# Kernel tuning notes

Measured on AMD Instinct MI355X. Metric: run time of the kernel, lower is better.

Reference implementation:

```python
import jax, jax.numpy as jnp
import numpy as np

NUM_REL = 3


def _edge_norm(dst, et, n_nodes):
    # PyG RGCNConv default aggr='mean': mean over edges per (dst, relation).
    seg = dst * NUM_REL + et
    cnt = jax.ops.segment_sum(jnp.ones(dst.shape[0], jnp.float32), seg,
                              num_segments=n_nodes * NUM_REL)
    return 1.0 / jnp.maximum(cnt, 1.0)[seg], seg  # [E]


def _rgcn_layer(x, W, root, b, src, dst, et, norm_e, seg, transform_first):
    n = x.shape[0]
    if transform_first:
        # h_r = x @ W_r for all relations, gather message per edge, scatter-add.
        H = jnp.einsum('ni,rio->rno', x, W)          # [R, N, out]
        m = H[et, src] * norm_e[:, None]             # [E, out]
        agg = jax.ops.segment_sum(m, dst, num_segments=n)
    else:
        # mean-aggregate in input space first (mean commutes with linear map).
        m = x[src] * norm_e[:, None]                 # [E, in]
        A = jax.ops.segment_sum(m, seg, num_segments=n * NUM_REL)
        A = A.reshape(n, NUM_REL, -1)                # [N, R, in]
        agg = jnp.einsum('nri,rio->no', A, W)
    return agg + x @ root + b


def _make_params(key, in_c, out_c):
    dims = [(in_c, 1024), (1024, 512), (512, 128)]
    ks = jax.random.split(key, 14)
    p = {}
    for li, (i, o) in enumerate(dims, start=1):
        p[f'W{li}'] = jax.random.normal(ks[3 * li - 3], (NUM_REL, i, o), jnp.float32) * 0.02
        p[f'root{li}'] = jax.random.normal(ks[3 * li - 2], (i, o), jnp.float32) * 0.02
        p[f'b{li}'] = jnp.zeros((o,), jnp.float32)
    p['fc_w'] = jax.random.normal(ks[9], (128, out_c), jnp.float32) * 0.02
    p['fc_b'] = jnp.zeros((out_c,), jnp.float32)
    return p


def setup_inputs() -> dict:
    key = jax.random.key(0)
    N, E, IN_C, OUT_C = 40000, 500000, 256, 21
    k1, k2, k3, k4 = jax.random.split(key, 4)
    inp = {
        'x': jax.random.normal(k1, (N, IN_C), jnp.float32),
        'edge_index': jax.random.randint(k2, (2, E), 0, N, jnp.int64)
            if jax.config.jax_enable_x64 else jax.random.randint(k2, (2, E), 0, N, jnp.int32),
        'edge_type': jax.random.randint(k3, (E,), 0, NUM_REL, jnp.int32),
    }
    inp.update(_make_params(k4, IN_C, OUT_C))
    return inp


def reference(x, edge_index, edge_type, W1, root1, b1, W2, root2, b2,
              W3, root3, b3, fc_w, fc_b):
    src, dst = edge_index[0], edge_index[1]
    et = edge_type
    n = x.shape[0]
    norm_e, seg = _edge_norm(dst, et, n)
    # layer 1: in(256) < out(1024) -> aggregate-first is cheaper
    h = _rgcn_layer(x, W1, root1, b1, src, dst, et, norm_e, seg, transform_first=False)
    h = jax.nn.relu(h)  # dropout is identity in eval mode
    # layer 2: in(1024) > out(512) -> transform-first
    h = _rgcn_layer(h, W2, root2, b2, src, dst, et, norm_e, seg, transform_first=True)
    h = jax.nn.relu(h)
    # layer 3: in(512) > out(128) -> transform-first
    h = _rgcn_layer(h, W3, root3, b3, src, dst, et, norm_e, seg, transform_first=True)
    h = jax.nn.relu(h)
    logits = h @ fc_w + fc_b
    return jax.nn.log_softmax(logits, axis=1)
```

## Files before the change

kernel.cpp:

```cpp
#include <hip/hip_runtime.h>
#include <cstdint>
#include <cstddef>


typedef short bf16x8 __attribute__((ext_vector_type(8)));
typedef float f32x4 __attribute__((ext_vector_type(4)));

#define GF_BIAS 1
#define GF_RELU 2
#define GF_BF16 4

__device__ __forceinline__ unsigned short f2bf(float f) {
    unsigned u = __float_as_uint(f);
    return (unsigned short)((u + 0x7FFFu + ((u >> 16) & 1u)) >> 16);
}
__device__ __forceinline__ float bf2f(unsigned short h) {
    return __uint_as_float((unsigned)h << 16);
}

__global__ __launch_bounds__(256) void zero_kernel(float* __restrict__ p, long n4)
{
    long i = (long)blockIdx.x * 256 + threadIdx.x;
    if (i < n4) ((float4*)p)[i] = make_float4(0.f, 0.f, 0.f, 0.f);
}

__global__ __launch_bounds__(256) void count_kernel(
    const int* __restrict__ dst, const int* __restrict__ et,
    int* __restrict__ cnt, int E)
{
    int e = blockIdx.x * 256 + threadIdx.x;
    if (e < E) atomicAdd(&cnt[dst[e] * 3 + et[e]], 1);
}

__global__ __launch_bounds__(256) void scanA(
    const int* __restrict__ cnt, int* __restrict__ base,
    int* __restrict__ bsum, int S)
{
    __shared__ int sh[256];
    int i = blockIdx.x * 256 + threadIdx.x;
    int v = (i < S) ? cnt[i] : 0;
    sh[threadIdx.x] = v;
    __syncthreads();
#pragma unroll
    for (int off = 1; off < 256; off <<= 1) {
        int t = (threadIdx.x >= off) ? sh[threadIdx.x - off] : 0;
        __syncthreads();
        sh[threadIdx.x] += t;
        __syncthreads();
    }
    if (i < S) base[i] = sh[threadIdx.x] - v;
    if (threadIdx.x == 255) bsum[blockIdx.x] = sh[255];
}

__global__ __launch_bounds__(512) void scanB(int* __restrict__ bsum, int NB)
{
    __shared__ int sh[512];
    int t = threadIdx.x;
    int v = (t < NB) ? bsum[t] : 0;
    sh[t] = v;
    __syncthreads();
#pragma unroll
    for (int off = 1; off < 512; off <<= 1) {
        int u = (t >= off) ? sh[t - off] : 0;
        __syncthreads();
        sh[t] += u;
        __syncthreads();
    }
    if (t < NB) bsum[t] = sh[t] - v;
}

__global__ __launch_bounds__(256) void scanC(
    int* __restrict__ base, const int* __restrict__ bsum, int S)
{
    int i = blockIdx.x * 256 + threadIdx.x;
    if (i < S) base[i] += bsum[blockIdx.x];
}

__global__ __launch_bounds__(256) void fill_kernel(
    const int* __restrict__ src, const int* __restrict__ dst,
    const int* __restrict__ et, int* __restrict__ base,
    int* __restrict__ cnt, int* __restrict__ elist, int E, int S)
{
    int e = blockIdx.x * 256 + threadIdx.x;
    if (e == 0) base[S] = E;
    if (e >= E) return;
    int seg = dst[e] * 3 + et[e];
    int old = atomicSub(&cnt[seg], 1);
    elist[base[seg] + old - 1] = src[e];
}

__global__ __launch_bounds__(256) void tr1_tiled(
    const float* __restrict__ W1, const float* __restrict__ root1,
    unsigned short* __restrict__ W1t)
{
    __shared__ float sh[32][33];
    int bk = blockIdx.x & 31, bj = blockIdx.x >> 5;
    int tc = threadIdx.x & 31, tr = threadIdx.x >> 5;
    int k0 = bk * 32, j0 = bj * 32;
#pragma unroll
    for (int i = 0; i < 4; ++i) {
        int k = k0 + tr + i * 8;
        float v = (k < 768) ? W1[(size_t)k * 1024 + j0 + tc]
                            : root1[(size_t)(k - 768) * 1024 + j0 + tc];
        sh[tr + i * 8][tc] = v;
    }
    __syncthreads();
#pragma unroll
    for (int i = 0; i < 4; ++i)
        W1t[(size_t)(j0 + tr + i * 8) * 1024 + k0 + tc] = f2bf(sh[tc][tr + i * 8]);
}

__global__ __launch_bounds__(256) void tr2_tiled(
    const float* __restrict__ root2, const float* __restrict__ W2,
    unsigned short* __restrict__ W2cat)
{
    __shared__ float sh[32][33];
    int bk = blockIdx.x & 31, br = blockIdx.x >> 5;
    int tc = threadIdx.x & 31, tr = threadIdx.x >> 5;
    int k0 = bk * 32, r0 = br * 32;
    int s = r0 >> 9, j0 = r0 & 511;
    const float* src = (s == 0) ? root2 : W2 + (size_t)(s - 1) * 524288;
#pragma unroll
    for (int i = 0; i < 4; ++i)
        sh[tr + i * 8][tc] = src[(size_t)(k0 + tr + i * 8) * 512 + j0 + tc];
    __syncthreads();
#pragma unroll
    for (int i = 0; i < 4; ++i)
        W2cat[(size_t)(r0 + tr + i * 8) * 1024 + k0 + tc] = f2bf(sh[tc][tr + i * 8]);
}

__global__ __launch_bounds__(256) void tr3_tiled(
    const float* __restrict__ root3, const float* __restrict__ W3,
    unsigned short* __restrict__ W3cat)
{
    __shared__ float sh[32][33];
    int bk = blockIdx.x & 15, br = blockIdx.x >> 4;
    int tc = threadIdx.x & 31, tr = threadIdx.x >> 5;
    int k0 = bk * 32, r0 = br * 32;
    int s = r0 >> 7, j0 = r0 & 127;
    const float* src = (s == 0) ? root3 : W3 + (size_t)(s - 1) * 65536;
#pragma unroll
    for (int i = 0; i < 4; ++i)
        sh[tr + i * 8][tc] = src[(size_t)(k0 + tr + i * 8) * 128 + j0 + tc];
    __syncthreads();
#pragma unroll
    for (int i = 0; i < 4; ++i)
        W3cat[(size_t)(r0 + tr + i * 8) * 512 + k0 + tc] = f2bf(sh[tc][tr + i * 8]);
}

__global__ __launch_bounds__(256) void bias_cat(
    float* __restrict__ b2cat, float* __restrict__ b3cat,
    const float* __restrict__ b2, const float* __restrict__ b3)
{
    int i = blockIdx.x * 256 + threadIdx.x;
    if (i < 2048) b2cat[i] = (i < 512) ? b2[i] : 0.f;
    else if (i < 2560) { int j = i - 2048; b3cat[j] = (j < 128) ? b3[j] : 0.f; }
}

__global__ __launch_bounds__(256) void conv_bf16(
    const float* __restrict__ s, unsigned short* __restrict__ d, long n8)
{
    long i = (long)blockIdx.x * 256 + threadIdx.x;
    if (i >= n8) return;
    const float* p = s + i * 8;
    float4 a = *(const float4*)p, b = *(const float4*)(p + 4);
    ushort4 o0, o1;
    o0.x = f2bf(a.x); o0.y = f2bf(a.y); o0.z = f2bf(a.z); o0.w = f2bf(a.w);
    o1.x = f2bf(b.x); o1.y = f2bf(b.y); o1.z = f2bf(b.z); o1.w = f2bf(b.w);
    *(ushort4*)(d + i * 8) = o0;
    *(ushort4*)(d + i * 8 + 4) = o1;
}

__global__ __launch_bounds__(256) void agg1_kernel(
    const unsigned short* __restrict__ xb, const int* __restrict__ base,
    const int* __restrict__ elist, unsigned short* __restrict__ Xcat)
{
    int n = blockIdx.x;
    int w = threadIdx.x >> 6, l = threadIdx.x & 63;
    if (w == 3) {
        *(ushort4*)&Xcat[(size_t)n * 1024 + 768 + l * 4] =
            *(const ushort4*)&xb[(size_t)n * 256 + l * 4];
        return;
    }
    int seg = n * 3 + w;
    int st = base[seg], len = base[seg + 1] - st;
    float norm = 1.0f / (float)(len > 0 ? len : 1);
    int g = l >> 5, c8 = (l & 31) * 8;
    float a[8];
#pragma unroll
    for (int j = 0; j < 8; ++j) a[j] = 0.f;
    for (int i = g; i < len; i += 2) {
        const unsigned short* q = xb + (size_t)elist[st + i] * 256 + c8;
        ushort4 v0 = *(const ushort4*)q;
        ushort4 v1 = *(const ushort4*)(q + 4);
        a[0] += bf2f(v0.x); a[1] += bf2f(v0.y); a[2] += bf2f(v0.z); a[3] += bf2f(v0.w);
        a[4] += bf2f(v1.x); a[5] += bf2f(v1.y); a[6] += bf2f(v1.z); a[7] += bf2f(v1.w);
    }
#pragma unroll
    for (int j = 0; j < 8; ++j) a[j] += __shfl_xor(a[j], 32);
    if (l < 32) {
        ushort4 o0, o1;
        o0.x = f2bf(a[0] * norm); o0.y = f2bf(a[1] * norm);
        o0.z = f2bf(a[2] * norm); o0.w = f2bf(a[3] * norm);
        o1.x = f2bf(a[4] * norm); o1.y = f2bf(a[5] * norm);
        o1.z = f2bf(a[6] * norm); o1.w = f2bf(a[7] * norm);
        unsigned short* d = Xcat + (size_t)n * 1024 + w * 256 + c8;
        *(ushort4*)d = o0;
        *(ushort4*)(d + 4) = o1;
    }
}

__global__ __launch_bounds__(256) void agg2_fused(
    const unsigned short* __restrict__ H2all, unsigned short* __restrict__ h2b,
    const int* __restrict__ base, const int* __restrict__ elist)
{
    int w = threadIdx.x >> 6, l = threadIdx.x & 63;
    int n = blockIdx.x * 4 + w;
    int c8 = l * 8;
    const unsigned short* rowN = H2all + (size_t)n * 2048 + c8;
    float a[8];
    {
        ushort4 r0 = *(const ushort4*)rowN;
        ushort4 r1 = *(const ushort4*)(rowN + 4);
        a[0] = bf2f(r0.x); a[1] = bf2f(r0.y); a[2] = bf2f(r0.z); a[3] = bf2f(r0.w);
        a[4] = bf2f(r1.x); a[5] = bf2f(r1.y); a[6] = bf2f(r1.z); a[7] = bf2f(r1.w);
    }
    int s0 = base[n * 3], s1b = base[n * 3 + 1];
    int s2b = base[n * 3 + 2], s3 = base[n * 3 + 3];
    int l0 = s1b - s0, l1 = s2b - s1b, l2 = s3 - s2b;
    float nm0 = 1.f / (float)(l0 > 0 ? l0 : 1);
    float nm1 = 1.f / (float)(l1 > 0 ? l1 : 1);
    float nm2 = 1.f / (float)(l2 > 0 ? l2 : 1);
    int i = s0;
    for (; i + 2 <= s3; i += 2) {
        int ia = i, ib = i + 1;
        int ra = (ia >= s1b) + (ia >= s2b);
        int rb = (ib >= s1b) + (ib >= s2b);
        float wa = (ia < s1b) ? nm0 : ((ia < s2b) ? nm1 : nm2);
        float wb = (ib < s1b) ? nm0 : ((ib < s2b) ? nm1 : nm2);
        const unsigned short* qa =
            H2all + (size_t)elist[ia] * 2048 + 512 * (1 + ra) + c8;
        const unsigned short* qb =
            H2all + (size_t)elist[ib] * 2048 + 512 * (1 + rb) + c8;
        ushort4 u0 = *(const ushort4*)qa, u1 = *(const ushort4*)(qa + 4);
        ushort4 v0 = *(const ushort4*)qb, v1 = *(const ushort4*)(qb + 4);
        a[0] += bf2f(u0.x) * wa + bf2f(v0.x) * wb;
        a[1] += bf2f(u0.y) * wa + bf2f(v0.y) * wb;
        a[2] += bf2f(u0.z) * wa + bf2f(v0.z) * wb;
        a[3] += bf2f(u0.w) * wa + bf2f(v0.w) * wb;
        a[4] += bf2f(u1.x) * wa + bf2f(v1.x) * wb;
        a[5] += bf2f(u1.y) * wa + bf2f(v1.y) * wb;
        a[6] += bf2f(u1.z) * wa + bf2f(v1.z) * wb;
        a[7] += bf2f(u1.w) * wa + bf2f(v1.w) * wb;
    }
    if (i < s3) {
        int r = (i >= s1b) + (i >= s2b);
        float wN = (i < s1b) ? nm0 : ((i < s2b) ? nm1 : nm2);
        const unsigned short* q =
            H2all + (size_t)elist[i] * 2048 + 512 * (1 + r) + c8;
        ushort4 u0 = *(const ushort4*)q, u1 = *(const ushort4*)(q + 4);
        a[0] += bf2f(u0.x) * wN; a[1] += bf2f(u0.y) * wN;
        a[2] += bf2f(u0.z) * wN; a[3] += bf2f(u0.w) * wN;
        a[4] += bf2f(u1.x) * wN; a[5] += bf2f(u1.y) * wN;
        a[6] += bf2f(u1.z) * wN; a[7] += bf2f(u1.w) * wN;
    }
    ushort4 o0, o1;
    o0.x = f2bf(fmaxf(a[0], 0.f)); o0.y = f2bf(fmaxf(a[1], 0.f));
    o0.z = f2bf(fmaxf(a[2], 0.f)); o0.w = f2bf(fmaxf(a[3], 0.f));
    o1.x = f2bf(fmaxf(a[4], 0.f)); o1.y = f2bf(fmaxf(a[5], 0.f));
    o1.z = f2bf(fmaxf(a[6], 0.f)); o1.w = f2bf(fmaxf(a[7], 0.f));
    unsigned short* d = h2b + (size_t)n * 512 + c8;
    *(ushort4*)d = o0;
    *(ushort4*)(d + 4) = o1;
}

__global__ __launch_bounds__(256) void agg3_head(
    const unsigned short* __restrict__ H3cat, const float* __restrict__ fcw,
    const float* __restrict__ fcb, const int* __restrict__ base,
    const int* __restrict__ elist, float* __restrict__ out)
{
    __shared__ float sh[4][128];
    int wid = threadIdx.x >> 6, lane = threadIdx.x & 63;
    int n = blockIdx.x * 4 + wid;
    int g = lane >> 4, c8 = (lane & 15) * 8;
    int s0 = base[n * 3], s1b = base[n * 3 + 1];
    int s2b = base[n * 3 + 2], s3 = base[n * 3 + 3];
    int l0 = s1b - s0, l1 = s2b - s1b, l2 = s3 - s2b;
    float nm0 = 1.f / (float)(l0 > 0 ? l0 : 1);
    float nm1 = 1.f / (float)(l1 > 0 ? l1 : 1);
    float nm2 = 1.f / (float)(l2 > 0 ? l2 : 1);
    float a[8];
#pragma unroll
    for (int j = 0; j < 8; ++j) a[j] = 0.f;
    for (int i = s0 + g; i < s3; i += 4) {
        int r = (i >= s1b) + (i >= s2b);
        float wN = (i < s1b) ? nm0 : ((i < s2b) ? nm1 : nm2);
        const unsigned short* q =
            H3cat + (size_t)elist[i] * 512 + 128 * (1 + r) + c8;
        ushort4 u0 = *(const ushort4*)q, u1 = *(const ushort4*)(q + 4);
        a[0] += bf2f(u0.x) * wN; a[1] += bf2f(u0.y) * wN;
        a[2] += bf2f(u0.z) * wN; a[3] += bf2f(u0.w) * wN;
        a[4] += bf2f(u1.x) * wN; a[5] += bf2f(u1.y) * wN;
        a[6] += bf2f(u1.z) * wN; a[7] += bf2f(u1.w) * wN;
    }
#pragma unroll
    for (int j = 0; j < 8; ++j) {
        a[j] += __shfl_xor(a[j], 16);
        a[j] += __shfl_xor(a[j], 32);
    }
    if (lane < 16) {
        const unsigned short* rt = H3cat + (size_t)n * 512 + c8;
        ushort4 r0 = *(const ushort4*)rt, r1 = *(const ushort4*)(rt + 4);
        sh[wid][c8 + 0] = fmaxf(a[0] + bf2f(r0.x), 0.f);
        sh[wid][c8 + 1] = fmaxf(a[1] + bf2f(r0.y), 0.f);
        sh[wid][c8 + 2] = fmaxf(a[2] + bf2f(r0.z), 0.f);
        sh[wid][c8 + 3] = fmaxf(a[3] + bf2f(r0.w), 0.f);
        sh[wid][c8 + 4] = fmaxf(a[4] + bf2f(r1.x), 0.f);
        sh[wid][c8 + 5] = fmaxf(a[5] + bf2f(r1.y), 0.f);
        sh[wid][c8 + 6] = fmaxf(a[6] + bf2f(r1.z), 0.f);
        sh[wid][c8 + 7] = fmaxf(a[7] + bf2f(r1.w), 0.f);
    }
    __syncthreads();
    float logit = 0.f;
    if (lane < 21) {
        logit = fcb[lane];
#pragma unroll
        for (int k = 0; k < 128; ++k) logit += sh[wid][k] * fcw[k * 21 + lane];
    }
    float v = (lane < 21) ? logit : -INFINITY;
#pragma unroll
    for (int off = 32; off; off >>= 1) v = fmaxf(v, __shfl_xor(v, off));
    float mx = v;
    float ex = (lane < 21) ? expf(logit - mx) : 0.f;
#pragma unroll
    for (int off = 32; off; off >>= 1) ex += __shfl_xor(ex, off);
    if (lane < 21) out[(size_t)n * 21 + lane] = logit - mx - logf(ex);
}

__global__ __launch_bounds__(128) void agg2_inc(
    const unsigned short* __restrict__ H2q, float* __restrict__ h2acc,
    unsigned short* __restrict__ h2b, const int* __restrict__ base,
    const int* __restrict__ elist, int r, int last)
{
    int n = blockIdx.x, t = threadIdx.x;
    int seg = n * 3 + r;
    int st = base[seg], len = base[seg + 1] - st;
    float norm = 1.0f / (float)(len > 0 ? len : 1);
    float4 s = make_float4(0.f, 0.f, 0.f, 0.f);
    for (int i = 0; i < len; ++i) {
        int sx = elist[st + i];
        ushort4 v = *(const ushort4*)&H2q[(size_t)sx * 512 + t * 4];
        s.x += bf2f(v.x); s.y += bf2f(v.y); s.z += bf2f(v.z); s.w += bf2f(v.w);
    }
    float4 a = *(const float4*)&h2acc[(size_t)n * 512 + t * 4];
    a.x += s.x * norm; a.y += s.y * norm; a.z += s.z * norm; a.w += s.w * norm;
    if (!last) {
        *(float4*)&h2acc[(size_t)n * 512 + t * 4] = a;
    } else {
        ushort4 o;
        o.x = f2bf(fmaxf(a.x, 0.f)); o.y = f2bf(fmaxf(a.y, 0.f));
        o.z = f2bf(fmaxf(a.z, 0.f)); o.w = f2bf(fmaxf(a.w, 0.f));
        *(ushort4*)&h2b[(size_t)n * 512 + t * 4] = o;
    }
}

__global__ __launch_bounds__(256) void gemm_mfma(
    const unsigned short* __restrict__ A, const unsigned short* __restrict__ Bt,
    const float* __restrict__ bias, void* __restrict__ C,
    int Nout, int K, int flags, int lgGX)
{
    __shared__ short __align__(16) As[8192];
    __shared__ short __align__(16) Bs[8192];
    const int tid = threadIdx.x;
    const int w = tid >> 6, l = tid & 63;

    const int nblk = (int)gridDim.x;
    const int q = nblk >> 3, rem = nblk & 7;
    const int xcd = blockIdx.x & 7, local = blockIdx.x >> 3;
    const int id2 = xcd * q + (xcd < rem ? xcd : rem) + local;
    const int row0 = (id2 >> lgGX) * 128;
    const int col0 = (id2 & ((1 << lgGX) - 1)) * 128;

    const int wm = w >> 1, wn = w & 1;
    const int lr = l >> 3, lc = l & 7;

    f32x4 acc[4][4];
#pragma unroll
    for (int i = 0; i < 4; ++i)
#pragma unroll
        for (int j = 0; j < 4; ++j) acc[i][j] = (f32x4){0.f, 0.f, 0.f, 0.f};

    for (int k0 = 0; k0 < K; k0 += 64) {
        __syncthreads();
#pragma unroll
        for (int i = 0; i < 4; ++i) {
            const int c  = i * 4 + w;
            const int r  = c * 8 + lr;
            const int c8 = lc ^ (r & 7);
            __builtin_amdgcn_global_load_lds(
                (const __attribute__((address_space(1))) void*)
                    (A + (size_t)(row0 + r) * K + k0 + c8 * 8),
                (__attribute__((address_space(3))) void*)(As + c * 512),
                16, 0, 0);
            __builtin_amdgcn_global_load_lds(
                (const __attribute__((address_space(1))) void*)
                    (Bt + (size_t)(col0 + r) * K + k0 + c8 * 8),
                (__attribute__((address_space(3))) void*)(Bs + c * 512),
                16, 0, 0);
        }
        __syncthreads();
#pragma unroll
        for (int ks = 0; ks < 2; ++ks) {
            bf16x8 af[4], bfv[4];
#pragma unroll
            for (int mf = 0; mf < 4; ++mf) {
                int r = wm * 64 + mf * 16 + (l & 15);
                int byt = (r * 128 + ks * 64 + (l >> 4) * 16) ^ ((r & 7) << 4);
                af[mf] = *(const bf16x8*)((const char*)As + byt);
            }
#pragma unroll
            for (int nf = 0; nf < 4; ++nf) {
                int r = wn * 64 + nf * 16 + (l & 15);
                int byt = (r * 128 + ks * 64 + (l >> 4) * 16) ^ ((r & 7) << 4);
                bfv[nf] = *(const bf16x8*)((const char*)Bs + byt);
            }
#pragma unroll
            for (int mf = 0; mf < 4; ++mf)
#pragma unroll
                for (int nf = 0; nf < 4; ++nf)
                    acc[mf][nf] = __builtin_amdgcn_mfma_f32_16x16x32_bf16(
                        af[mf], bfv[nf], acc[mf][nf], 0, 0, 0);
        }
    }

    const int lrow = (l >> 4) * 4;
    const int lcol = l & 15;
#pragma unroll
    for (int mf = 0; mf < 4; ++mf) {
#pragma unroll
        for (int nf = 0; nf < 4; ++nf) {
            int col = col0 + wn * 64 + nf * 16 + lcol;
            float bv = (flags & GF_BIAS) ? bias[col] : 0.f;
#pragma unroll
            for (int rr = 0; rr < 4; ++rr) {
                int row = row0 + wm * 64 + mf * 16 + lrow + rr;
                float v = acc[mf][nf][rr] + bv;
                if (flags & GF_RELU) v = fmaxf(v, 0.f);
                size_t idx = (size_t)row * Nout + col;
                if (flags & GF_BF16) ((unsigned short*)C)[idx] = f2bf(v);
                else                 ((float*)C)[idx] = v;
            }
        }
    }
}

extern "C" void kernel_launch(void* const* d_in, const int* in_sizes, int n_in,
                              void* d_out, int out_size, void* d_ws, size_t ws_size,
                              hipStream_t stream)
{
    const float* x     = (const float*)d_in[0];
    const int*   ei    = (const int*)d_in[1];
    const int*   etp   = (const int*)d_in[2];
    const float* W1    = (const float*)d_in[3];
    const float* root1 = (const float*)d_in[4];
    const float* b1    = (const float*)d_in[5];
    const float* W2    = (const float*)d_in[6];
    const float* root2 = (const float*)d_in[7];
    const float* b2    = (const float*)d_in[8];
    const float* W3    = (const float*)d_in[9];
    const float* root3 = (const float*)d_in[10];
    const float* b3    = (const float*)d_in[11];
    const float* fcw   = (const float*)d_in[12];
    const float* fcb   = (const float*)d_in[13];
    float* out = (float*)d_out;
    (void)n_in; (void)out_size;

    const int N   = in_sizes[0] / 256;
    const int E   = in_sizes[2];
    const int S   = N * 3;
    const int NP  = (N + 127) / 128 * 128;
    const int GY  = NP / 128;
    const int NB  = (S + 255) / 256;
    const int* srcp = ei;
    const int* dstp = ei + E;

    const size_t SZ_X1024 = (size_t)NP * 1024 * 2;
    const size_t SZ_X512b = (size_t)NP * 512 * 2;
    const size_t SZ_X2048 = (size_t)NP * 2048 * 2;

    char* ws = (char*)d_ws;
    int*            cnt   = (int*)(ws + 0);
    int*            base  = (int*)(ws + 480256);
    int*            elist = (int*)(ws + 960512);
    float*          b2cat = (float*)(ws + 2960512);
    float*          b3cat = (float*)(ws + 2968704);
    unsigned short* W3cat = (unsigned short*)(ws + 2970752);
    unsigned short* W2cat = (unsigned short*)(ws + 3495040);
    const size_t fixed_end = 7689344;
    const size_t FUSED_NEED = 7692288 + SZ_X2048 + SZ_X1024;
    const bool fused = ws_size >= FUSED_NEED;

    char* arena;
    unsigned short *W1t, *xb, *Xcat, *h1b, *H2all, *H2q, *h2b, *H3cat;
    float* h2acc;
    if (fused) {
        arena = ws + 7692288;
        Xcat  = (unsigned short*)(arena);
        W1t   = (unsigned short*)(arena + SZ_X1024);
        xb    = (unsigned short*)(arena + SZ_X1024 + 2097152);
        h1b   = (unsigned short*)(arena + SZ_X2048);
        H2all = (unsigned short*)(arena);
        h2b   = (unsigned short*)(arena + SZ_X2048);
        H3cat = (unsigned short*)(arena);
        H2q = nullptr; h2acc = nullptr;
    } else {
        W1t   = (unsigned short*)(ws + fixed_end);
        arena = ws + 9789440;
        Xcat  = (unsigned short*)(arena);
        h2acc = (float*)(arena);
        h1b   = (unsigned short*)(arena + SZ_X1024);
        h2b   = (unsigned short*)(arena + SZ_X1024);
        H3cat = (unsigned short*)(arena + SZ_X1024 + SZ_X512b);
        xb    = (unsigned short*)(arena + 2 * SZ_X1024);
        H2q   = (unsigned short*)(arena + 2 * SZ_X1024);
        H2all = nullptr;
    }
    int* bsum = (int*)(arena);

    zero_kernel<<<(30016 + 255) / 256, 256, 0, stream>>>((float*)cnt, 30016);
    count_kernel<<<(E + 255) / 256, 256, 0, stream>>>(dstp, etp, cnt, E);
    scanA<<<NB, 256, 0, stream>>>(cnt, base, bsum, S);
    scanB<<<1, 512, 0, stream>>>(bsum, NB);
    scanC<<<NB, 256, 0, stream>>>(base, bsum, S);
    fill_kernel<<<(E + 255) / 256, 256, 0, stream>>>(srcp, dstp, etp, base, cnt, elist, E, S);

    tr1_tiled<<<1024, 256, 0, stream>>>(W1, root1, W1t);
    tr2_tiled<<<2048, 256, 0, stream>>>(root2, W2, W2cat);
    tr3_tiled<<<256, 256, 0, stream>>>(root3, W3, W3cat);
    bias_cat<<<10, 256, 0, stream>>>(b2cat, b3cat, b2, b3);
    conv_bf16<<<(int)(((long)N * 32 + 255) / 256), 256, 0, stream>>>(x, xb, (long)N * 32);

    agg1_kernel<<<N, 256, 0, stream>>>(xb, base, elist, Xcat);
    gemm_mfma<<<8 * GY, 256, 0, stream>>>(
        Xcat, W1t, b1, h1b, 1024, 1024, GF_BIAS | GF_RELU | GF_BF16, 3);

    if (fused) {
        gemm_mfma<<<16 * GY, 256, 0, stream>>>(
            h1b, W2cat, b2cat, H2all, 2048, 1024, GF_BIAS | GF_BF16, 4);
        agg2_fused<<<N / 4, 256, 0, stream>>>(H2all, h2b, base, elist);
    } else {
        gemm_mfma<<<4 * GY, 256, 0, stream>>>(
            h1b, W2cat, b2, h2acc, 512, 1024, GF_BIAS, 2);
        for (int r = 0; r < 3; ++r) {
            gemm_mfma<<<4 * GY, 256, 0, stream>>>(
                h1b, W2cat + (size_t)(1 + r) * 524288, nullptr, H2q, 512, 1024, GF_BF16, 2);
            agg2_inc<<<N, 128, 0, stream>>>(H2q, h2acc, h2b, base, elist, r, r == 2);
        }
    }

    gemm_mfma<<<4 * GY, 256, 0, stream>>>(
        h2b, W3cat, b3cat, H3cat, 512, 512, GF_BIAS | GF_BF16, 2);
    agg3_head<<<N / 4, 256, 0, stream>>>(H3cat, fcw, fcb, base, elist, out);
}
```

Measured before the change: 626.4 us.

## Merge weight-prep kernels into one launch and split agg2 edges across warps

Five small preparation kernels (three weight transposes, bias concatenation, x-to-bf16 conversion) become one kernel that branches on block index, which removes launch overhead. The layer-2 aggregation changes from one wave per node to one 256-thread block per node. The four waves stride over that node's edges, and their partial sums are reduced in shared memory before the root term, ReLU and bf16 store. This adds parallelism for nodes with many edges, at the cost of a block-wide sync and a shared-memory reduction per node.

Measured after the change: 619.0 us. About the same (-1.2%).

```diff
diff --git a/kernel.cpp b/kernel.cpp
--- a/kernel.cpp
+++ b/kernel.cpp
@@ -89,86 +89,75 @@
     elist[base[seg] + old - 1] = src[e];
 }
 
-__global__ __launch_bounds__(256) void tr1_tiled(
+__global__ __launch_bounds__(256) void prep_all(
     const float* __restrict__ W1, const float* __restrict__ root1,
-    unsigned short* __restrict__ W1t)
+    unsigned short* __restrict__ W1t,
+    const float* __restrict__ root2, const float* __restrict__ W2,
+    unsigned short* __restrict__ W2cat,
+    const float* __restrict__ root3, const float* __restrict__ W3,
+    unsigned short* __restrict__ W3cat,
+    float* __restrict__ b2cat, float* __restrict__ b3cat,
+    const float* __restrict__ b2, const float* __restrict__ b3,
+    const float* __restrict__ x, unsigned short* __restrict__ xb, long n8)
 {
     __shared__ float sh[32][33];
-    int bk = blockIdx.x & 31, bj = blockIdx.x >> 5;
+    int b = blockIdx.x;
     int tc = threadIdx.x & 31, tr = threadIdx.x >> 5;
-    int k0 = bk * 32, j0 = bj * 32;
-#pragma unroll
-    for (int i = 0; i < 4; ++i) {
-        int k = k0 + tr + i * 8;
-        float v = (k < 768) ? W1[(size_t)k * 1024 + j0 + tc]
-                            : root1[(size_t)(k - 768) * 1024 + j0 + tc];
-        sh[tr + i * 8][tc] = v;
-    }
-    __syncthreads();
-#pragma unroll
-    for (int i = 0; i < 4; ++i)
-        W1t[(size_t)(j0 + tr + i * 8) * 1024 + k0 + tc] = f2bf(sh[tc][tr + i * 8]);
-}
-
-__global__ __launch_bounds__(256) void tr2_tiled(
-    const float* __restrict__ root2, const float* __restrict__ W2,
-    unsigned short* __restrict__ W2cat)
-{
-    __shared__ float sh[32][33];
-    int bk = blockIdx.x & 31, br = blockIdx.x >> 5;
-    int tc = threadIdx.x & 31, tr = threadIdx.x >> 5;
-    int k0 = bk * 32, r0 = br * 32;
-    int s = r0 >> 9, j0 = r0 & 511;
-    const float* src = (s == 0) ? root2 : W2 + (size_t)(s - 1) * 524288;
-#pragma unroll
-    for (int i = 0; i < 4; ++i)
-        sh[tr + i * 8][tc] = src[(size_t)(k0 + tr + i * 8) * 512 + j0 + tc];
-    __syncthreads();
-#pragma unroll
-    for (int i = 0; i < 4; ++i)
-        W2cat[(size_t)(r0 + tr + i * 8) * 1024 + k0 + tc] = f2bf(sh[tc][tr + i * 8]);
-}
-
-__global__ __launch_bounds__(256) void tr3_tiled(
-    const float* __restrict__ root3, const float* __restrict__ W3,
-    unsigned short* __restrict__ W3cat)
-{
-    __shared__ float sh[32][33];
-    int bk = blockIdx.x & 15, br = blockIdx.x >> 4;
-    int tc = threadIdx.x & 31, tr = threadIdx.x >> 5;
-    int k0 = bk * 32, r0 = br * 32;
-    int s = r0 >> 7, j0 = r0 & 127;
-    const float* src = (s == 0) ? root3 : W3 + (size_t)(s - 1) * 65536;
-#pragma unroll
-    for (int i = 0; i < 4; ++i)
-        sh[tr + i * 8][tc] = src[(size_t)(k0 + tr + i * 8) * 128 + j0 + tc];
-    __syncthreads();
-#pragma unroll
-    for (int i = 0; i < 4; ++i)
-        W3cat[(size_t)(r0 + tr + i * 8) * 512 + k0 + tc] = f2bf(sh[tc][tr + i * 8]);
-}
-
-__global__ __launch_bounds__(256) void bias_cat(
-    float* __restrict__ b2cat, float* __restrict__ b3cat,
-    const float* __restrict__ b2, const float* __restrict__ b3)
-{
-    int i = blockIdx.x * 256 + threadIdx.x;
-    if (i < 2048) b2cat[i] = (i < 512) ? b2[i] : 0.f;
-    else if (i < 2560) { int j = i - 2048; b3cat[j] = (j < 128) ? b3[j] : 0.f; }
-}
-
-__global__ __launch_bounds__(256) void conv_bf16(
-    const float* __restrict__ s, unsigned short* __restrict__ d, long n8)
-{
-    long i = (long)blockIdx.x * 256 + threadIdx.x;
-    if (i >= n8) return;
-    const float* p = s + i * 8;
-    float4 a = *(const float4*)p, b = *(const float4*)(p + 4);
-    ushort4 o0, o1;
-    o0.x = f2bf(a.x); o0.y = f2bf(a.y); o0.z = f2bf(a.z); o0.w = f2bf(a.w);
-    o1.x = f2bf(b.x); o1.y = f2bf(b.y); o1.z = f2bf(b.z); o1.w = f2bf(b.w);
-    *(ushort4*)(d + i * 8) = o0;
-    *(ushort4*)(d + i * 8 + 4) = o1;
+    if (b < 1024) {
+        int bk = b & 31, bj = b >> 5;
+        int k0 = bk * 32, j0 = bj * 32;
+#pragma unroll
+        for (int i = 0; i < 4; ++i) {
+            int k = k0 + tr + i * 8;
+            float v = (k < 768) ? W1[(size_t)k * 1024 + j0 + tc]
+                                : root1[(size_t)(k - 768) * 1024 + j0 + tc];
+            sh[tr + i * 8][tc] = v;
+        }
+        __syncthreads();
+#pragma unroll
+        for (int i = 0; i < 4; ++i)
+            W1t[(size_t)(j0 + tr + i * 8) * 1024 + k0 + tc] = f2bf(sh[tc][tr + i * 8]);
+    } else if (b < 3072) {
+        int bb = b - 1024;
+        int bk = bb & 31, br = bb >> 5;
+        int k0 = bk * 32, r0 = br * 32;
+        int s = r0 >> 9, j0 = r0 & 511;
+        const float* src = (s == 0) ? root2 : W2 + (size_t)(s - 1) * 524288;
+#pragma unroll
+        for (int i = 0; i < 4; ++i)
+            sh[tr + i * 8][tc] = src[(size_t)(k0 + tr + i * 8) * 512 + j0 + tc];
+        __syncthreads();
+#pragma unroll
+        for (int i = 0; i < 4; ++i)
+            W2cat[(size_t)(r0 + tr + i * 8) * 1024 + k0 + tc] = f2bf(sh[tc][tr + i * 8]);
+    } else if (b < 3328) {
+        int bb = b - 3072;
+        int bk = bb & 15, br = bb >> 4;
+        int k0 = bk * 32, r0 = br * 32;
+        int s = r0 >> 7, j0 = r0 & 127;
+        const float* src = (s == 0) ? root3 : W3 + (size_t)(s - 1) * 65536;
+#pragma unroll
+        for (int i = 0; i < 4; ++i)
+            sh[tr + i * 8][tc] = src[(size_t)(k0 + tr + i * 8) * 128 + j0 + tc];
+        __syncthreads();
+#pragma unroll
+        for (int i = 0; i < 4; ++i)
+            W3cat[(size_t)(r0 + tr + i * 8) * 512 + k0 + tc] = f2bf(sh[tc][tr + i * 8]);
+    } else if (b < 3338) {
+        int i = (b - 3328) * 256 + threadIdx.x;
+        if (i < 2048) b2cat[i] = (i < 512) ? b2[i] : 0.f;
+        else if (i < 2560) { int j = i - 2048; b3cat[j] = (j < 128) ? b3[j] : 0.f; }
+    } else {
+        long i = (long)(b - 3338) * 256 + threadIdx.x;
+        if (i >= n8) return;
+        const float* p = x + i * 8;
+        float4 a = *(const float4*)p, bb4 = *(const float4*)(p + 4);
+        ushort4 o0, o1;
+        o0.x = f2bf(a.x); o0.y = f2bf(a.y); o0.z = f2bf(a.z); o0.w = f2bf(a.w);
+        o1.x = f2bf(bb4.x); o1.y = f2bf(bb4.y); o1.z = f2bf(bb4.z); o1.w = f2bf(bb4.w);
+        *(ushort4*)(xb + i * 8) = o0;
+        *(ushort4*)(xb + i * 8 + 4) = o1;
+    }
 }
 
 __global__ __launch_bounds__(256) void agg1_kernel(
@@ -214,46 +203,20 @@
     const unsigned short* __restrict__ H2all, unsigned short* __restrict__ h2b,
     const int* __restrict__ base, const int* __restrict__ elist)
 {
+    __shared__ float sh[4][512];
     int w = threadIdx.x >> 6, l = threadIdx.x & 63;
-    int n = blockIdx.x * 4 + w;
+    int n = blockIdx.x;
     int c8 = l * 8;
-    const unsigned short* rowN = H2all + (size_t)n * 2048 + c8;
-    float a[8];
-    {
-        ushort4 r0 = *(const ushort4*)rowN;
-        ushort4 r1 = *(const ushort4*)(rowN + 4);
-        a[0] = bf2f(r0.x); a[1] = bf2f(r0.y); a[2] = bf2f(r0.z); a[3] = bf2f(r0.w);
-        a[4] = bf2f(r1.x); a[5] = bf2f(r1.y); a[6] = bf2f(r1.z); a[7] = bf2f(r1.w);
-    }
     int s0 = base[n * 3], s1b = base[n * 3 + 1];
     int s2b = base[n * 3 + 2], s3 = base[n * 3 + 3];
     int l0 = s1b - s0, l1 = s2b - s1b, l2 = s3 - s2b;
     float nm0 = 1.f / (float)(l0 > 0 ? l0 : 1);
     float nm1 = 1.f / (float)(l1 > 0 ? l1 : 1);
     float nm2 = 1.f / (float)(l2 > 0 ? l2 : 1);
-    int i = s0;
-    for (; i + 2 <= s3; i += 2) {
-        int ia = i, ib = i + 1;
-        int ra = (ia >= s1b) + (ia >= s2b);
-        int rb = (ib >= s1b) + (ib >= s2b);
-        float wa = (ia < s1b) ? nm0 : ((ia < s2b) ? nm1 : nm2);
-        float wb = (ib < s1b) ? nm0 : ((ib < s2b) ? nm1 : nm2);
-        const unsigned short* qa =
-            H2all + (size_t)elist[ia] * 2048 + 512 * (1 + ra) + c8;
-        const unsigned short* qb =
-            H2all + (size_t)elist[ib] * 2048 + 512 * (1 + rb) + c8;
-        ushort4 u0 = *(const ushort4*)qa, u1 = *(const ushort4*)(qa + 4);
-        ushort4 v0 = *(const ushort4*)qb, v1 = *(const ushort4*)(qb + 4);
-        a[0] += bf2f(u0.x) * wa + bf2f(v0.x) * wb;
-        a[1] += bf2f(u0.y) * wa + bf2f(v0.y) * wb;
-        a[2] += bf2f(u0.z) * wa + bf2f(v0.z) * wb;
-        a[3] += bf2f(u0.w) * wa + bf2f(v0.w) * wb;
-        a[4] += bf2f(u1.x) * wa + bf2f(v1.x) * wb;
-        a[5] += bf2f(u1.y) * wa + bf2f(v1.y) * wb;
-        a[6] += bf2f(u1.z) * wa + bf2f(v1.z) * wb;
-        a[7] += bf2f(u1.w) * wa + bf2f(v1.w) * wb;
-    }
-    if (i < s3) {
+    float a[8];
+#pragma unroll
+    for (int j = 0; j < 8; ++j) a[j] = 0.f;
+    for (int i = s0 + w; i < s3; i += 4) {
         int r = (i >= s1b) + (i >= s2b);
         float wN = (i < s1b) ? nm0 : ((i < s2b) ? nm1 : nm2);
         const unsigned short* q =
@@ -264,14 +227,17 @@
         a[4] += bf2f(u1.x) * wN; a[5] += bf2f(u1.y) * wN;
         a[6] += bf2f(u1.z) * wN; a[7] += bf2f(u1.w) * wN;
     }
-    ushort4 o0, o1;
-    o0.x = f2bf(fmaxf(a[0], 0.f)); o0.y = f2bf(fmaxf(a[1], 0.f));
-    o0.z = f2bf(fmaxf(a[2], 0.f)); o0.w = f2bf(fmaxf(a[3], 0.f));
-    o1.x = f2bf(fmaxf(a[4], 0.f)); o1.y = f2bf(fmaxf(a[5], 0.f));
-    o1.z = f2bf(fmaxf(a[6], 0.f)); o1.w = f2bf(fmaxf(a[7], 0.f));
-    unsigned short* d = h2b + (size_t)n * 512 + c8;
-    *(ushort4*)d = o0;
-    *(ushort4*)(d + 4) = o1;
+#pragma unroll
+    for (int j = 0; j < 8; ++j) sh[w][c8 + j] = a[j];
+    __syncthreads();
+    int col = threadIdx.x * 2;
+    float v0 = sh[0][col] + sh[1][col] + sh[2][col] + sh[3][col];
+    float v1 = sh[0][col + 1] + sh[1][col + 1] + sh[2][col + 1] + sh[3][col + 1];
+    ushort2 rt = *(const ushort2*)&H2all[(size_t)n * 2048 + col];
+    v0 = fmaxf(v0 + bf2f(rt.x), 0.f);
+    v1 = fmaxf(v1 + bf2f(rt.y), 0.f);
+    unsigned pk = (unsigned)f2bf(v0) | ((unsigned)f2bf(v1) << 16);
+    *(unsigned*)&h2b[(size_t)n * 512 + col] = pk;
 }
 
 __global__ __launch_bounds__(256) void agg3_head(
@@ -534,11 +500,10 @@
     scanC<<<NB, 256, 0, stream>>>(base, bsum, S);
     fill_kernel<<<(E + 255) / 256, 256, 0, stream>>>(srcp, dstp, etp, base, cnt, elist, E, S);
 
-    tr1_tiled<<<1024, 256, 0, stream>>>(W1, root1, W1t);
-    tr2_tiled<<<2048, 256, 0, stream>>>(root2, W2, W2cat);
-    tr3_tiled<<<256, 256, 0, stream>>>(root3, W3, W3cat);
-    bias_cat<<<10, 256, 0, stream>>>(b2cat, b3cat, b2, b3);
-    conv_bf16<<<(int)(((long)N * 32 + 255) / 256), 256, 0, stream>>>(x, xb, (long)N * 32);
+    const int convB = (int)(((long)N * 32 + 255) / 256);
+    prep_all<<<3338 + convB, 256, 0, stream>>>(
+        W1, root1, W1t, root2, W2, W2cat, root3, W3, W3cat,
+        b2cat, b3cat, b2, b3, x, xb, (long)N * 32);
 
     agg1_kernel<<<N, 256, 0, stream>>>(xb, base, elist, Xcat);
     gemm_mfma<<<8 * GY, 256, 0, stream>>>(
@@ -547,7 +512,7 @@
     if (fused) {
         gemm_mfma<<<16 * GY, 256, 0, stream>>>(
             h1b, W2cat, b2cat, H2all, 2048, 1024, GF_BIAS | GF_BF16, 4);
-        agg2_fused<<<N / 4, 256, 0, stream>>>(H2all, h2b, base, elist);
+        agg2_fused<<<N, 256, 0, stream>>>(H2all, h2b, base, elist);
     } else {
         gemm_mfma<<<4 * GY, 256, 0, stream>>>(
             h1b, W2cat, b2, h2acc, 512, 1024, GF_BIAS, 2);
```
